# Kernel tuning notes

Hardware: AMD Instinct MI355X
Metric: run time of the kernel (lower is better)

## Reference

```python
import jax, jax.numpy as jnp
import numpy as np

B, F, H, M, T = 4096, 256, 256, 3, 30
IN0 = 2 + F  # GRU layer-0 input: concat(current_pos[2], context[F])


def setup_inputs() -> dict:
    key = jax.random.key(0)
    ks = jax.random.split(key, 15)
    s = 0.05
    rn = lambda k, shp: jax.random.normal(k, shp, jnp.float32) * s
    return dict(
        context=jax.random.normal(ks[0], (B, F), jnp.float32),
        mp_w1=rn(ks[1], (64, F)), mp_b1=rn(ks[2], (64,)),
        mp_w2=rn(ks[3], (M, 64)), mp_b2=rn(ks[4], (M,)),
        w_ih0=rn(ks[5], (M, 3 * H, IN0)), w_hh0=rn(ks[6], (M, 3 * H, H)),
        b_ih0=rn(ks[7], (M, 3 * H)), b_hh0=rn(ks[8], (M, 3 * H)),
        w_ih1=rn(ks[9], (M, 3 * H, H)), w_hh1=rn(ks[10], (M, 3 * H, H)),
        b_ih1=rn(ks[11], (M, 3 * H)), b_hh1=rn(ks[12], (M, 3 * H)),
        out_w=rn(ks[13], (M, 2, H)), out_b=rn(ks[14], (M, 2)),
        num_future_steps=T,
    )


def _gru_cell(x, h, w_ih, w_hh, b_ih, b_hh):
    # PyTorch GRU cell, gate order (r, z, n)
    gx = x @ w_ih.T + b_ih  # (B, 3H)
    gh = h @ w_hh.T + b_hh  # (B, 3H)
    xr, xz, xn = jnp.split(gx, 3, axis=-1)
    hr, hz, hn = jnp.split(gh, 3, axis=-1)
    r = jax.nn.sigmoid(xr + hr)
    z = jax.nn.sigmoid(xz + hz)
    n = jnp.tanh(xn + r * hn)
    return (1.0 - z) * n + z * h


def reference(context, mp_w1, mp_b1, mp_w2, mp_b2,
              w_ih0, w_hh0, b_ih0, b_hh0,
              w_ih1, w_hh1, b_ih1, b_hh1,
              out_w, out_b, num_future_steps):
    mode_logits = jax.nn.relu(context @ mp_w1.T + mp_b1) @ mp_w2.T + mp_b2
    mode_probs = jax.nn.softmax(mode_logits, axis=-1)  # (B, M)

    def decode_mode(wi0, wh0, bi0, bh0, wi1, wh1, bi1, bh1, ow, ob):
        def step(carry, _):
            h0, h1, pos = carry
            x = jnp.concatenate([pos, context], axis=-1)  # (B, 2+F)
            h0n = _gru_cell(x, h0, wi0, wh0, bi0, bh0)
            h1n = _gru_cell(h0n, h1, wi1, wh1, bi1, bh1)
            delta = h1n @ ow.T + ob  # (B, 2)
            return (h0n, h1n, delta), delta

        pos0 = jnp.zeros((context.shape[0], 2), context.dtype)
        # hidden = context.unsqueeze(0).repeat(2,1,1): both layers init to context
        (_, _, _), deltas = jax.lax.scan(step, (context, context, pos0), None,
                                          length=num_future_steps)
        # deltas: (T, B, 2) -> (B, T, 2), cumulative sum over time
        return jnp.cumsum(deltas.transpose(1, 0, 2), axis=1)

    trajs = jax.vmap(decode_mode)(w_ih0, w_hh0, b_ih0, b_hh0,
                                  w_ih1, w_hh1, b_ih1, b_hh1,
                                  out_w, out_b)  # (M, B, T, 2)
    trajectories = trajs.transpose(1, 0, 2, 3)  # (B, M, T, 2)
    return trajectories, mode_probs
```

## Files before the change

kernel.cpp:

```cpp
#include <hip/hip_runtime.h>


typedef __attribute__((ext_vector_type(8))) short bf16x8;
typedef __attribute__((ext_vector_type(4))) float f32x4;

__device__ __forceinline__ short f2bf(float f) {
    unsigned u = __builtin_bit_cast(unsigned, f);
    unsigned r = (u + 0x7fffu + ((u >> 16) & 1u)) >> 16;
    return (short)r;
}
__device__ __forceinline__ float bf2f(short s) {
    unsigned u = ((unsigned)(unsigned short)s) << 16;
    return __builtin_bit_cast(float, u);
}
__device__ __forceinline__ float fast_sigmoid(float x) {
    x = fminf(fmaxf(x, -30.f), 30.f);
    float e = __builtin_amdgcn_exp2f(x * -1.442695041f);
    return __builtin_amdgcn_rcpf(1.f + e);
}
__device__ __forceinline__ float fast_tanh(float x) {
    x = fminf(fmaxf(x, -15.f), 15.f);
    float e = __builtin_amdgcn_exp2f(x * -2.885390082f);
    return (1.f - e) * __builtin_amdgcn_rcpf(1.f + e);
}

__global__ void prep_kernel(const float* __restrict__ w_ih0,
                            const float* __restrict__ w_hh0,
                            const float* __restrict__ w_ih1,
                            const float* __restrict__ w_hh1,
                            short* __restrict__ ws) {
    int bid = blockIdx.x;
    int L = threadIdx.x;
    const float* src;
    int srcRowLen, colBase, m, w, ks, t;
    if (bid < 1152) {
        int idx = bid, mw = idx / 48, blk = idx % 48;
        m = mw / 8; w = mw % 8;
        if (blk < 32) { ks = blk >> 2; t = blk & 3; }
        else { int q = blk - 32; ks = q >> 1; t = 4 + (q & 1); }
        src = w_hh0 + (size_t)m * 768 * 256; srcRowLen = 256; colBase = 0;
    } else if (bid < 3456) {
        int idx = bid - 1152, mw = idx / 96, blk = idx % 96;
        m = mw / 8; w = mw % 8;
        int half;
        if (blk < 64) { half = blk >> 5; ks = (blk >> 2) & 7; t = blk & 3; }
        else { int q = blk - 64; half = q >> 4; ks = (q >> 1) & 7; t = 4 + (q & 1); }
        src = (half ? w_hh1 : w_ih1) + (size_t)m * 768 * 256;
        srcRowLen = 256; colBase = 0;
    } else {
        int idx = bid - 3456, mw = idx / 48, blk = idx % 48;
        m = mw / 8; w = mw % 8; ks = blk / 6; t = blk % 6;
        src = w_ih0 + (size_t)m * 768 * 258; srcRowLen = 258; colBase = 2;
    }
    int row = (t >> 1) * 256 + 32 * w + (t & 1) * 16 + (L & 15);
    int col0 = colBase + ks * 32 + (L >> 4) * 8;
    short* dst = ws + (size_t)bid * 512 + L * 8;
    const float* s = src + (size_t)row * srcRowLen + col0;
#pragma unroll
    for (int j = 0; j < 8; ++j) dst[j] = f2bf(s[j]);
}

__global__ __launch_bounds__(256) void modeprobs_kernel(
    const float* __restrict__ ctx, const float* __restrict__ w1,
    const float* __restrict__ b1, const float* __restrict__ w2,
    const float* __restrict__ b2, float* __restrict__ out,
    long probs_off) {
    __shared__ float w1s[64 * 256];
    int tid = threadIdx.x;
    int j = tid & 63;
    int rsub = tid >> 6;
#pragma unroll
    for (int i = 0; i < 64; ++i) w1s[tid + i * 256] = w1[tid + i * 256];
    float b1v = b1[j];
    float w2v0 = w2[j], w2v1 = w2[64 + j], w2v2 = w2[128 + j];
    float b20 = b2[0], b21 = b2[1], b22 = b2[2];
    __syncthreads();
    for (int c = 0; c < 16; ++c) {
        int brow = blockIdx.x * 64 + c * 4 + rsub;
        const float* crow = ctx + (size_t)brow * 256;
        float accv = b1v;
#pragma unroll 8
        for (int k = 0; k < 256; ++k) {
            int kk = (k + j) & 255;
            accv += w1s[j * 256 + kk] * crow[kk];
        }
        float h = fmaxf(accv, 0.f);
        float l0 = h * w2v0, l1 = h * w2v1, l2 = h * w2v2;
#pragma unroll
        for (int s = 1; s < 64; s <<= 1) {
            l0 += __shfl_xor(l0, s);
            l1 += __shfl_xor(l1, s);
            l2 += __shfl_xor(l2, s);
        }
        if (j == 0) {
            l0 += b20; l1 += b21; l2 += b22;
            float mx = fmaxf(l0, fmaxf(l1, l2));
            float e0 = __builtin_amdgcn_exp2f((l0 - mx) * 1.442695041f);
            float e1 = __builtin_amdgcn_exp2f((l1 - mx) * 1.442695041f);
            float e2 = __builtin_amdgcn_exp2f((l2 - mx) * 1.442695041f);
            float inv = 1.f / (e0 + e1 + e2);
            out[probs_off + (size_t)brow * 3 + 0] = e0 * inv;
            out[probs_off + (size_t)brow * 3 + 1] = e1 * inv;
            out[probs_off + (size_t)brow * 3 + 2] = e2 * inv;
        }
    }
}

__global__ __launch_bounds__(512, 2) void decoder_kernel(
    const float* __restrict__ context,
    const float* __restrict__ w_ih0_f,
    const float* __restrict__ b_ih0, const float* __restrict__ b_hh0,
    const float* __restrict__ b_ih1, const float* __restrict__ b_hh1,
    const float* __restrict__ out_w, const float* __restrict__ out_b,
    const short* __restrict__ ws, float* __restrict__ out,
    const int* __restrict__ pT, int ntiles) {
    __shared__ short ctxS[64 * 264];
    __shared__ short h0a[64 * 264], h0b[64 * 264];
    __shared__ short h1s[64 * 264];
    __shared__ float posD[128];
    __shared__ float owl[512];
    __shared__ float cwp0[768], cwp1[768];
    __shared__ float cbA[512];
    __shared__ float cbXn[256];
    __shared__ float cbh0n[256];
    __shared__ float cb1A[512];
    __shared__ float cb1X[256];
    __shared__ float cb1H[256];

    const int bid = blockIdx.x;
    const int xcd = bid & 7, slot = bid >> 3;
    int mode, xl, nx;
    if (xcd < 3)      { mode = 0; xl = xcd;     nx = 3; }
    else if (xcd < 6) { mode = 1; xl = xcd - 3; nx = 3; }
    else              { mode = 2; xl = xcd - 6; nx = 2; }
    const int g = slot * nx + xl;
    if (g >= ntiles) return;
    const int m = mode;
    const int b0 = g * 64;

    const int T = *pT;
    const int tid = threadIdx.x;
    const int lane = tid & 63, w = tid >> 6;
    const int lr = lane & 15, quad = lane >> 4;

    if (tid < 128) posD[tid] = 0.f;
    owl[tid] = out_w[m * 512 + tid];
    if (tid < 512) {
        cbA[tid] = b_ih0[m * 768 + tid] + b_hh0[m * 768 + tid];
        cb1A[tid] = b_ih1[m * 768 + tid] + b_hh1[m * 768 + tid];
    }
    if (tid < 256) {
        cbXn[tid] = b_ih0[m * 768 + 512 + tid];
        cbh0n[tid] = b_hh0[m * 768 + 512 + tid];
        cb1X[tid] = b_ih1[m * 768 + 512 + tid];
        cb1H[tid] = b_hh1[m * 768 + 512 + tid];
    }
    for (int c = tid; c < 768; c += 512) {
        cwp0[c] = w_ih0_f[((size_t)m * 768 + c) * 258 + 0];
        cwp1[c] = w_ih0_f[((size_t)m * 768 + c) * 258 + 1];
    }
#pragma unroll
    for (int i = 0; i < 32; ++i) {
        int idx = tid + i * 512;
        int r = idx >> 8, k = idx & 255;
        short v = f2bf(context[(size_t)(b0 + r) * 256 + k]);
        ctxS[r * 264 + k] = v;
        h0a[r * 264 + k] = v;
        h1s[r * 264 + k] = v;
    }
    const float ob0v = out_b[m * 2 + 0], ob1v = out_b[m * 2 + 1];

    const short* p0w = ws + ((size_t)(m * 8 + w) * 48) * 512 + lane * 8;
    const short* p1w = ws + (size_t)1152 * 512 + ((size_t)(m * 8 + w) * 96) * 512 + lane * 8;
    const short* pcw = ws + (size_t)3456 * 512 + ((size_t)(m * 8 + w) * 48) * 512 + lane * 8;

    const int cA = 32 * w + lr;
    const int cB = 32 * w + 16 + lr;

    __syncthreads();

    float cum0 = 0.f, cum1 = 0.f;

    for (int st = 0; st < T; ++st) {
        const short* h0c = (st & 1) ? h0b : h0a;
        short* h0n_ = (st & 1) ? h0a : h0b;

        {
            f32x4 arz[4][4], axn[2][4], ahn[2][4];
#pragma unroll
            for (int rt = 0; rt < 4; ++rt)
#pragma unroll
                for (int r = 0; r < 4; ++r) {
                    int row = rt * 16 + quad * 4 + r;
                    float px = posD[row * 2], py = posD[row * 2 + 1];
#pragma unroll
                    for (int t = 0; t < 4; ++t) {
                        int c = (t >> 1) * 256 + ((t & 1) ? cB : cA);
                        arz[t][rt][r] = cbA[c] + px * cwp0[c] + py * cwp1[c];
                    }
#pragma unroll
                    for (int nt = 0; nt < 2; ++nt) {
                        int cn = nt ? cB : cA;
                        axn[nt][rt][r] = cbXn[cn] + px * cwp0[512 + cn] +
                                         py * cwp1[512 + cn];
                        ahn[nt][rt][r] = cbh0n[cn];
                    }
                }
            const short* bpc = pcw;
            const short* bp0rz = p0w;
            const short* bp0n = p0w + 32 * 512;
#pragma unroll 1
            for (int ks = 0; ks < 8; ++ks) {
                bf16x8 ac[4], ah[4];
#pragma unroll
                for (int rt = 0; rt < 4; ++rt) {
                    ac[rt] = *reinterpret_cast<const bf16x8*>(
                        ctxS + (rt * 16 + lr) * 264 + ks * 32 + quad * 8);
                    ah[rt] = *reinterpret_cast<const bf16x8*>(
                        h0c + (rt * 16 + lr) * 264 + ks * 32 + quad * 8);
                }
#pragma unroll
                for (int t = 0; t < 4; ++t) {
                    bf16x8 b = *reinterpret_cast<const bf16x8*>(bpc + t * 512);
#pragma unroll
                    for (int rt = 0; rt < 4; ++rt)
                        arz[t][rt] = __builtin_amdgcn_mfma_f32_16x16x32_bf16(
                            ac[rt], b, arz[t][rt], 0, 0, 0);
                }
#pragma unroll
                for (int nt = 0; nt < 2; ++nt) {
                    bf16x8 b = *reinterpret_cast<const bf16x8*>(bpc + (4 + nt) * 512);
#pragma unroll
                    for (int rt = 0; rt < 4; ++rt)
                        axn[nt][rt] = __builtin_amdgcn_mfma_f32_16x16x32_bf16(
                            ac[rt], b, axn[nt][rt], 0, 0, 0);
                }
#pragma unroll
                for (int t = 0; t < 4; ++t) {
                    bf16x8 b = *reinterpret_cast<const bf16x8*>(bp0rz + t * 512);
#pragma unroll
                    for (int rt = 0; rt < 4; ++rt)
                        arz[t][rt] = __builtin_amdgcn_mfma_f32_16x16x32_bf16(
                            ah[rt], b, arz[t][rt], 0, 0, 0);
                }
#pragma unroll
                for (int nt = 0; nt < 2; ++nt) {
                    bf16x8 b = *reinterpret_cast<const bf16x8*>(bp0n + nt * 512);
#pragma unroll
                    for (int rt = 0; rt < 4; ++rt)
                        ahn[nt][rt] = __builtin_amdgcn_mfma_f32_16x16x32_bf16(
                            ah[rt], b, ahn[nt][rt], 0, 0, 0);
                }
                bpc += 6 * 512;
                bp0rz += 4 * 512;
                bp0n += 2 * 512;
            }
#pragma unroll
            for (int nt = 0; nt < 2; ++nt) {
                int col = nt ? cB : cA;
#pragma unroll
                for (int rt = 0; rt < 4; ++rt)
#pragma unroll
                    for (int r = 0; r < 4; ++r) {
                        int row = rt * 16 + quad * 4 + r;
                        float rr = fast_sigmoid(arz[nt][rt][r]);
                        float zz = fast_sigmoid(arz[2 + nt][rt][r]);
                        float nn =
                            fast_tanh(axn[nt][rt][r] + rr * ahn[nt][rt][r]);
                        float hold = bf2f(h0c[row * 264 + col]);
                        h0n_[row * 264 + col] = f2bf((1.f - zz) * nn + zz * hold);
                    }
            }
        }
        __syncthreads();

        {
            f32x4 arz[4][4], axn[2][4], ahn[2][4];
#pragma unroll
            for (int rt = 0; rt < 4; ++rt)
#pragma unroll
                for (int r = 0; r < 4; ++r) {
#pragma unroll
                    for (int t = 0; t < 4; ++t) {
                        int c = (t >> 1) * 256 + ((t & 1) ? cB : cA);
                        arz[t][rt][r] = cb1A[c];
                    }
#pragma unroll
                    for (int nt = 0; nt < 2; ++nt) {
                        int cn = nt ? cB : cA;
                        axn[nt][rt][r] = cb1X[cn];
                        ahn[nt][rt][r] = cb1H[cn];
                    }
                }
            const short* bq0 = p1w;
            const short* bq1 = p1w + 32 * 512;
            const short* bx = p1w + 64 * 512;
            const short* bh = p1w + 80 * 512;
#pragma unroll 1
            for (int ks = 0; ks < 8; ++ks) {
                bf16x8 a0[4], a1[4];
#pragma unroll
                for (int rt = 0; rt < 4; ++rt) {
                    a0[rt] = *reinterpret_cast<const bf16x8*>(
                        h0n_ + (rt * 16 + lr) * 264 + ks * 32 + quad * 8);
                    a1[rt] = *reinterpret_cast<const bf16x8*>(
                        h1s + (rt * 16 + lr) * 264 + ks * 32 + quad * 8);
                }
#pragma unroll
                for (int t = 0; t < 4; ++t) {
                    bf16x8 b = *reinterpret_cast<const bf16x8*>(bq0 + t * 512);
#pragma unroll
                    for (int rt = 0; rt < 4; ++rt)
                        arz[t][rt] = __builtin_amdgcn_mfma_f32_16x16x32_bf16(
                            a0[rt], b, arz[t][rt], 0, 0, 0);
                }
#pragma unroll
                for (int nt = 0; nt < 2; ++nt) {
                    bf16x8 b = *reinterpret_cast<const bf16x8*>(bx + nt * 512);
#pragma unroll
                    for (int rt = 0; rt < 4; ++rt)
                        axn[nt][rt] = __builtin_amdgcn_mfma_f32_16x16x32_bf16(
                            a0[rt], b, axn[nt][rt], 0, 0, 0);
                }
#pragma unroll
                for (int t = 0; t < 4; ++t) {
                    bf16x8 b = *reinterpret_cast<const bf16x8*>(bq1 + t * 512);
#pragma unroll
                    for (int rt = 0; rt < 4; ++rt)
                        arz[t][rt] = __builtin_amdgcn_mfma_f32_16x16x32_bf16(
                            a1[rt], b, arz[t][rt], 0, 0, 0);
                }
#pragma unroll
                for (int nt = 0; nt < 2; ++nt) {
                    bf16x8 b = *reinterpret_cast<const bf16x8*>(bh + nt * 512);
#pragma unroll
                    for (int rt = 0; rt < 4; ++rt)
                        ahn[nt][rt] = __builtin_amdgcn_mfma_f32_16x16x32_bf16(
                            a1[rt], b, ahn[nt][rt], 0, 0, 0);
                }
                bq0 += 4 * 512;
                bq1 += 4 * 512;
                bx += 2 * 512;
                bh += 2 * 512;
            }
            __syncthreads();
#pragma unroll
            for (int nt = 0; nt < 2; ++nt) {
                int col = nt ? cB : cA;
#pragma unroll
                for (int rt = 0; rt < 4; ++rt)
#pragma unroll
                    for (int r = 0; r < 4; ++r) {
                        int row = rt * 16 + quad * 4 + r;
                        float rr = fast_sigmoid(arz[nt][rt][r]);
                        float zz = fast_sigmoid(arz[2 + nt][rt][r]);
                        float nn =
                            fast_tanh(axn[nt][rt][r] + rr * ahn[nt][rt][r]);
                        float hold = bf2f(h1s[row * 264 + col]);
                        h1s[row * 264 + col] = f2bf((1.f - zz) * nn + zz * hold);
                    }
            }
        }
        __syncthreads();

        {
            int brow = tid >> 3, p = tid & 7;
            float d0 = 0.f, d1 = 0.f;
#pragma unroll
            for (int j = 0; j < 4; ++j) {
                int cb = ((p + brow) & 7) * 8 + j * 64;
                bf16x8 hv8 = *reinterpret_cast<const bf16x8*>(h1s + brow * 264 + cb);
#pragma unroll
                for (int i = 0; i < 8; ++i) {
                    float hv = bf2f(hv8[i]);
                    d0 += hv * owl[cb + i];
                    d1 += hv * owl[256 + cb + i];
                }
            }
            d0 += __shfl_xor(d0, 1); d0 += __shfl_xor(d0, 2); d0 += __shfl_xor(d0, 4);
            d1 += __shfl_xor(d1, 1); d1 += __shfl_xor(d1, 2); d1 += __shfl_xor(d1, 4);
            d0 += ob0v;
            d1 += ob1v;
            if (p == 0) {
                cum0 += d0;
                cum1 += d1;
                size_t o = (((size_t)(b0 + brow) * 3 + m) * (size_t)T + st) * 2;
                out[o] = cum0;
                out[o + 1] = cum1;
                posD[brow * 2] = d0;
                posD[brow * 2 + 1] = d1;
            }
        }
        __syncthreads();
    }
}

extern "C" void kernel_launch(void* const* d_in, const int* in_sizes, int n_in,
                              void* d_out, int out_size, void* d_ws, size_t ws_size,
                              hipStream_t stream) {
    const float* context = (const float*)d_in[0];
    const float* mp_w1 = (const float*)d_in[1];
    const float* mp_b1 = (const float*)d_in[2];
    const float* mp_w2 = (const float*)d_in[3];
    const float* mp_b2 = (const float*)d_in[4];
    const float* w_ih0 = (const float*)d_in[5];
    const float* w_hh0 = (const float*)d_in[6];
    const float* b_ih0 = (const float*)d_in[7];
    const float* b_hh0 = (const float*)d_in[8];
    const float* w_ih1 = (const float*)d_in[9];
    const float* w_hh1 = (const float*)d_in[10];
    const float* b_ih1 = (const float*)d_in[11];
    const float* b_hh1 = (const float*)d_in[12];
    const float* out_w = (const float*)d_in[13];
    const float* out_b = (const float*)d_in[14];
    const int* pT = (const int*)d_in[15];
    float* out = (float*)d_out;
    short* ws = (short*)d_ws;

    const int B = in_sizes[0] / 256;
    const int ntiles = B / 64;
    const long probs_off = (long)out_size - (long)B * 3;

    prep_kernel<<<4608, 64, 0, stream>>>(w_ih0, w_hh0, w_ih1, w_hh1, ws);
    modeprobs_kernel<<<B / 64, 256, 0, stream>>>(context, mp_w1, mp_b1, mp_w2,
                                                 mp_b2, out, probs_off);
    const int nslots = (ntiles + 1) / 2;
    decoder_kernel<<<8 * nslots, 512, 0, stream>>>(
        context, w_ih0, b_ih0, b_hh0, b_ih1, b_hh1, out_w, out_b, ws, out, pT,
        ntiles);
}
```

Baseline: 976.4 us.

## Split GRU gate GEMMs into r/z and n passes with double-buffered weight loads

Each GRU layer's fused K-loop, which kept r/z and n accumulators live together, is split into two passes. The r/z pass applies sigmoid right away and keeps the results as floats, then the n pass runs with only its own accumulators. Each pass double-buffers the global weight fragments so the next K-slice's B operands load while the current MFMAs run. This is meant to lower accumulator register pressure and hide global load latency, at the cost of reading the A operands from LDS twice per step and holding extra rv/zv registers.

```diff
diff --git a/kernel.cpp b/kernel.cpp
--- a/kernel.cpp
+++ b/kernel.cpp
@@ -106,6 +106,71 @@
     }
 }
 
+__device__ __forceinline__ void load_rz(bf16x8 (&bu)[8], const short* pX,
+                                        const short* pY, int offX, int offY) {
+#pragma unroll
+    for (int t = 0; t < 4; ++t) {
+        bu[t] = *reinterpret_cast<const bf16x8*>(pX + offX + t * 512);
+        bu[4 + t] = *reinterpret_cast<const bf16x8*>(pY + offY + t * 512);
+    }
+}
+__device__ __forceinline__ void mfma_rz(f32x4 (&acc)[4][4], const bf16x8 (&bu)[8],
+                                        const short* aP, const short* bP,
+                                        int kk, int lr, int quad) {
+    bf16x8 a0[4], a1[4];
+#pragma unroll
+    for (int rt = 0; rt < 4; ++rt) {
+        a0[rt] = *reinterpret_cast<const bf16x8*>(
+            aP + (rt * 16 + lr) * 264 + kk * 32 + quad * 8);
+        a1[rt] = *reinterpret_cast<const bf16x8*>(
+            bP + (rt * 16 + lr) * 264 + kk * 32 + quad * 8);
+    }
+#pragma unroll
+    for (int t = 0; t < 4; ++t)
+#pragma unroll
+        for (int rt = 0; rt < 4; ++rt)
+            acc[t][rt] = __builtin_amdgcn_mfma_f32_16x16x32_bf16(
+                a0[rt], bu[t], acc[t][rt], 0, 0, 0);
+#pragma unroll
+    for (int t = 0; t < 4; ++t)
+#pragma unroll
+        for (int rt = 0; rt < 4; ++rt)
+            acc[t][rt] = __builtin_amdgcn_mfma_f32_16x16x32_bf16(
+                a1[rt], bu[4 + t], acc[t][rt], 0, 0, 0);
+}
+__device__ __forceinline__ void load_n(bf16x8 (&bu)[4], const short* pX,
+                                       const short* pY, int offX, int offY) {
+#pragma unroll
+    for (int t = 0; t < 2; ++t) {
+        bu[t] = *reinterpret_cast<const bf16x8*>(pX + offX + t * 512);
+        bu[2 + t] = *reinterpret_cast<const bf16x8*>(pY + offY + t * 512);
+    }
+}
+__device__ __forceinline__ void mfma_n(f32x4 (&ax)[2][4], f32x4 (&ah)[2][4],
+                                       const bf16x8 (&bu)[4], const short* aP,
+                                       const short* bP, int kk, int lr, int quad) {
+    bf16x8 a0[4], a1[4];
+#pragma unroll
+    for (int rt = 0; rt < 4; ++rt) {
+        a0[rt] = *reinterpret_cast<const bf16x8*>(
+            aP + (rt * 16 + lr) * 264 + kk * 32 + quad * 8);
+        a1[rt] = *reinterpret_cast<const bf16x8*>(
+            bP + (rt * 16 + lr) * 264 + kk * 32 + quad * 8);
+    }
+#pragma unroll
+    for (int nt = 0; nt < 2; ++nt)
+#pragma unroll
+        for (int rt = 0; rt < 4; ++rt)
+            ax[nt][rt] = __builtin_amdgcn_mfma_f32_16x16x32_bf16(
+                a0[rt], bu[nt], ax[nt][rt], 0, 0, 0);
+#pragma unroll
+    for (int nt = 0; nt < 2; ++nt)
+#pragma unroll
+        for (int rt = 0; rt < 4; ++rt)
+            ah[nt][rt] = __builtin_amdgcn_mfma_f32_16x16x32_bf16(
+                a1[rt], bu[2 + nt], ah[nt][rt], 0, 0, 0);
+}
+
 __global__ __launch_bounds__(512, 2) void decoder_kernel(
     const float* __restrict__ context,
     const float* __restrict__ w_ih0_f,
@@ -155,9 +220,9 @@
         cb1X[tid] = b_ih1[m * 768 + 512 + tid];
         cb1H[tid] = b_hh1[m * 768 + 512 + tid];
     }
-    for (int c = tid; c < 768; c += 512) {
-        cwp0[c] = w_ih0_f[((size_t)m * 768 + c) * 258 + 0];
-        cwp1[c] = w_ih0_f[((size_t)m * 768 + c) * 258 + 1];
+    for (int cc = tid; cc < 768; cc += 512) {
+        cwp0[cc] = w_ih0_f[((size_t)m * 768 + cc) * 258 + 0];
+        cwp1[cc] = w_ih0_f[((size_t)m * 768 + cc) * 258 + 1];
     }
 #pragma unroll
     for (int i = 0; i < 32; ++i) {
@@ -173,6 +238,10 @@
     const short* p0w = ws + ((size_t)(m * 8 + w) * 48) * 512 + lane * 8;
     const short* p1w = ws + (size_t)1152 * 512 + ((size_t)(m * 8 + w) * 96) * 512 + lane * 8;
     const short* pcw = ws + (size_t)3456 * 512 + ((size_t)(m * 8 + w) * 48) * 512 + lane * 8;
+    const short* p0n = p0w + 32 * 512;
+    const short* p1x = p1w + 64 * 512;
+    const short* p1h = p1w + 80 * 512;
+    const short* p1q = p1w + 32 * 512;
 
     const int cA = 32 * w + lr;
     const int cB = 32 * w + 16 + lr;
@@ -185,8 +254,9 @@
         const short* h0c = (st & 1) ? h0b : h0a;
         short* h0n_ = (st & 1) ? h0a : h0b;
 
+        float rv[2][4][4], zv[2][4][4];
         {
-            f32x4 arz[4][4], axn[2][4], ahn[2][4];
+            f32x4 arz[4][4];
 #pragma unroll
             for (int rt = 0; rt < 4; ++rt)
 #pragma unroll
@@ -198,6 +268,38 @@
                         int c = (t >> 1) * 256 + ((t & 1) ? cB : cA);
                         arz[t][rt][r] = cbA[c] + px * cwp0[c] + py * cwp1[c];
                     }
+                }
+            {
+                bf16x8 bu0[8], bu1[8];
+                load_rz(bu0, pcw, p0w, 0, 0);
+#pragma unroll 1
+                for (int ks2 = 0; ks2 < 4; ++ks2) {
+                    int k0 = 2 * ks2, k1 = k0 + 1, k2 = k0 + 2;
+                    load_rz(bu1, pcw, p0w, k1 * 6 * 512, k1 * 4 * 512);
+                    mfma_rz(arz, bu0, ctxS, h0c, k0, lr, quad);
+                    if (ks2 < 3)
+                        load_rz(bu0, pcw, p0w, k2 * 6 * 512, k2 * 4 * 512);
+                    mfma_rz(arz, bu1, ctxS, h0c, k1, lr, quad);
+                }
+            }
+#pragma unroll
+            for (int nt = 0; nt < 2; ++nt)
+#pragma unroll
+                for (int rt = 0; rt < 4; ++rt)
+#pragma unroll
+                    for (int r = 0; r < 4; ++r) {
+                        rv[nt][rt][r] = fast_sigmoid(arz[nt][rt][r]);
+                        zv[nt][rt][r] = fast_sigmoid(arz[2 + nt][rt][r]);
+                    }
+        }
+        {
+            f32x4 axn[2][4], ahn[2][4];
+#pragma unroll
+            for (int rt = 0; rt < 4; ++rt)
+#pragma unroll
+                for (int r = 0; r < 4; ++r) {
+                    int row = rt * 16 + quad * 4 + r;
+                    float px = posD[row * 2], py = posD[row * 2 + 1];
 #pragma unroll
                     for (int nt = 0; nt < 2; ++nt) {
                         int cn = nt ? cB : cA;
@@ -206,54 +308,18 @@
                         ahn[nt][rt][r] = cbh0n[cn];
                     }
                 }
-            const short* bpc = pcw;
-            const short* bp0rz = p0w;
-            const short* bp0n = p0w + 32 * 512;
+            {
+                bf16x8 bu0[4], bu1[4];
+                load_n(bu0, pcw, p0n, 4 * 512, 0);
 #pragma unroll 1
-            for (int ks = 0; ks < 8; ++ks) {
-                bf16x8 ac[4], ah[4];
-#pragma unroll
-                for (int rt = 0; rt < 4; ++rt) {
-                    ac[rt] = *reinterpret_cast<const bf16x8*>(
-                        ctxS + (rt * 16 + lr) * 264 + ks * 32 + quad * 8);
-                    ah[rt] = *reinterpret_cast<const bf16x8*>(
-                        h0c + (rt * 16 + lr) * 264 + ks * 32 + quad * 8);
-                }
-#pragma unroll
-                for (int t = 0; t < 4; ++t) {
-                    bf16x8 b = *reinterpret_cast<const bf16x8*>(bpc + t * 512);
-#pragma unroll
-                    for (int rt = 0; rt < 4; ++rt)
-                        arz[t][rt] = __builtin_amdgcn_mfma_f32_16x16x32_bf16(
-                            ac[rt], b, arz[t][rt], 0, 0, 0);
-                }
-#pragma unroll
-                for (int nt = 0; nt < 2; ++nt) {
-                    bf16x8 b = *reinterpret_cast<const bf16x8*>(bpc + (4 + nt) * 512);
-#pragma unroll
-                    for (int rt = 0; rt < 4; ++rt)
-                        axn[nt][rt] = __builtin_amdgcn_mfma_f32_16x16x32_bf16(
-                            ac[rt], b, axn[nt][rt], 0, 0, 0);
-                }
-#pragma unroll
-                for (int t = 0; t < 4; ++t) {
-                    bf16x8 b = *reinterpret_cast<const bf16x8*>(bp0rz + t * 512);
-#pragma unroll
-                    for (int rt = 0; rt < 4; ++rt)
-                        arz[t][rt] = __builtin_amdgcn_mfma_f32_16x16x32_bf16(
-                            ah[rt], b, arz[t][rt], 0, 0, 0);
-                }
-#pragma unroll
-                for (int nt = 0; nt < 2; ++nt) {
-                    bf16x8 b = *reinterpret_cast<const bf16x8*>(bp0n + nt * 512);
-#pragma unroll
-                    for (int rt = 0; rt < 4; ++rt)
-                        ahn[nt][rt] = __builtin_amdgcn_mfma_f32_16x16x32_bf16(
-                            ah[rt], b, ahn[nt][rt], 0, 0, 0);
-                }
-                bpc += 6 * 512;
-                bp0rz += 4 * 512;
-                bp0n += 2 * 512;
+                for (int ks2 = 0; ks2 < 4; ++ks2) {
+                    int k0 = 2 * ks2, k1 = k0 + 1, k2 = k0 + 2;
+                    load_n(bu1, pcw, p0n, (k1 * 6 + 4) * 512, k1 * 2 * 512);
+                    mfma_n(axn, ahn, bu0, ctxS, h0c, k0, lr, quad);
+                    if (ks2 < 3)
+                        load_n(bu0, pcw, p0n, (k2 * 6 + 4) * 512, k2 * 2 * 512);
+                    mfma_n(axn, ahn, bu1, ctxS, h0c, k1, lr, quad);
+                }
             }
 #pragma unroll
             for (int nt = 0; nt < 2; ++nt) {
@@ -263,85 +329,75 @@
 #pragma unroll
                     for (int r = 0; r < 4; ++r) {
                         int row = rt * 16 + quad * 4 + r;
-                        float rr = fast_sigmoid(arz[nt][rt][r]);
-                        float zz = fast_sigmoid(arz[2 + nt][rt][r]);
-                        float nn =
-                            fast_tanh(axn[nt][rt][r] + rr * ahn[nt][rt][r]);
+                        float nn = fast_tanh(axn[nt][rt][r] +
+                                             rv[nt][rt][r] * ahn[nt][rt][r]);
                         float hold = bf2f(h0c[row * 264 + col]);
-                        h0n_[row * 264 + col] = f2bf((1.f - zz) * nn + zz * hold);
+                        h0n_[row * 264 + col] =
+                            f2bf((1.f - zv[nt][rt][r]) * nn +
+                                 zv[nt][rt][r] * hold);
                     }
             }
         }
         __syncthreads();
 
         {
-            f32x4 arz[4][4], axn[2][4], ahn[2][4];
+            f32x4 arz[4][4];
 #pragma unroll
             for (int rt = 0; rt < 4; ++rt)
 #pragma unroll
-                for (int r = 0; r < 4; ++r) {
+                for (int r = 0; r < 4; ++r)
 #pragma unroll
                     for (int t = 0; t < 4; ++t) {
                         int c = (t >> 1) * 256 + ((t & 1) ? cB : cA);
                         arz[t][rt][r] = cb1A[c];
                     }
+            {
+                bf16x8 bu0[8], bu1[8];
+                load_rz(bu0, p1w, p1q, 0, 0);
+#pragma unroll 1
+                for (int ks2 = 0; ks2 < 4; ++ks2) {
+                    int k0 = 2 * ks2, k1 = k0 + 1, k2 = k0 + 2;
+                    load_rz(bu1, p1w, p1q, k1 * 4 * 512, k1 * 4 * 512);
+                    mfma_rz(arz, bu0, h0n_, h1s, k0, lr, quad);
+                    if (ks2 < 3)
+                        load_rz(bu0, p1w, p1q, k2 * 4 * 512, k2 * 4 * 512);
+                    mfma_rz(arz, bu1, h0n_, h1s, k1, lr, quad);
+                }
+            }
+#pragma unroll
+            for (int nt = 0; nt < 2; ++nt)
+#pragma unroll
+                for (int rt = 0; rt < 4; ++rt)
+#pragma unroll
+                    for (int r = 0; r < 4; ++r) {
+                        rv[nt][rt][r] = fast_sigmoid(arz[nt][rt][r]);
+                        zv[nt][rt][r] = fast_sigmoid(arz[2 + nt][rt][r]);
+                    }
+        }
+        {
+            f32x4 axn[2][4], ahn[2][4];
+#pragma unroll
+            for (int rt = 0; rt < 4; ++rt)
+#pragma unroll
+                for (int r = 0; r < 4; ++r)
 #pragma unroll
                     for (int nt = 0; nt < 2; ++nt) {
                         int cn = nt ? cB : cA;
                         axn[nt][rt][r] = cb1X[cn];
                         ahn[nt][rt][r] = cb1H[cn];
                     }
-                }
-            const short* bq0 = p1w;
-            const short* bq1 = p1w + 32 * 512;
-            const short* bx = p1w + 64 * 512;
-            const short* bh = p1w + 80 * 512;
+            {
+                bf16x8 bu0[4], bu1[4];
+                load_n(bu0, p1x, p1h, 0, 0);
 #pragma unroll 1
-            for (int ks = 0; ks < 8; ++ks) {
-                bf16x8 a0[4], a1[4];
-#pragma unroll
-                for (int rt = 0; rt < 4; ++rt) {
-                    a0[rt] = *reinterpret_cast<const bf16x8*>(
-                        h0n_ + (rt * 16 + lr) * 264 + ks * 32 + quad * 8);
-                    a1[rt] = *reinterpret_cast<const bf16x8*>(
-                        h1s + (rt * 16 + lr) * 264 + ks * 32 + quad * 8);
-                }
-#pragma unroll
-                for (int t = 0; t < 4; ++t) {
-                    bf16x8 b = *reinterpret_cast<const bf16x8*>(bq0 + t * 512);
-#pragma unroll
-                    for (int rt = 0; rt < 4; ++rt)
-                        arz[t][rt] = __builtin_amdgcn_mfma_f32_16x16x32_bf16(
-                            a0[rt], b, arz[t][rt], 0, 0, 0);
-                }
-#pragma unroll
-                for (int nt = 0; nt < 2; ++nt) {
-                    bf16x8 b = *reinterpret_cast<const bf16x8*>(bx + nt * 512);
-#pragma unroll
-                    for (int rt = 0; rt < 4; ++rt)
-                        axn[nt][rt] = __builtin_amdgcn_mfma_f32_16x16x32_bf16(
-                            a0[rt], b, axn[nt][rt], 0, 0, 0);
-                }
-#pragma unroll
-                for (int t = 0; t < 4; ++t) {
-                    bf16x8 b = *reinterpret_cast<const bf16x8*>(bq1 + t * 512);
-#pragma unroll
-                    for (int rt = 0; rt < 4; ++rt)
-                        arz[t][rt] = __builtin_amdgcn_mfma_f32_16x16x32_bf16(
-                            a1[rt], b, arz[t][rt], 0, 0, 0);
-                }
-#pragma unroll
-                for (int nt = 0; nt < 2; ++nt) {
-                    bf16x8 b = *reinterpret_cast<const bf16x8*>(bh + nt * 512);
-#pragma unroll
-                    for (int rt = 0; rt < 4; ++rt)
-                        ahn[nt][rt] = __builtin_amdgcn_mfma_f32_16x16x32_bf16(
-                            a1[rt], b, ahn[nt][rt], 0, 0, 0);
-                }
-                bq0 += 4 * 512;
-                bq1 += 4 * 512;
-                bx += 2 * 512;
-                bh += 2 * 512;
+                for (int ks2 = 0; ks2 < 4; ++ks2) {
+                    int k0 = 2 * ks2, k1 = k0 + 1, k2 = k0 + 2;
+                    load_n(bu1, p1x, p1h, k1 * 2 * 512, k1 * 2 * 512);
+                    mfma_n(axn, ahn, bu0, h0n_, h1s, k0, lr, quad);
+                    if (ks2 < 3)
+                        load_n(bu0, p1x, p1h, k2 * 2 * 512, k2 * 2 * 512);
+                    mfma_n(axn, ahn, bu1, h0n_, h1s, k1, lr, quad);
+                }
             }
             __syncthreads();
 #pragma unroll
@@ -352,12 +408,12 @@
 #pragma unroll
                     for (int r = 0; r < 4; ++r) {
                         int row = rt * 16 + quad * 4 + r;
-                        float rr = fast_sigmoid(arz[nt][rt][r]);
-                        float zz = fast_sigmoid(arz[2 + nt][rt][r]);
-                        float nn =
-                            fast_tanh(axn[nt][rt][r] + rr * ahn[nt][rt][r]);
+                        float nn = fast_tanh(axn[nt][rt][r] +
+                                             rv[nt][rt][r] * ahn[nt][rt][r]);
                         float hold = bf2f(h1s[row * 264 + col]);
-                        h1s[row * 264 + col] = f2bf((1.f - zz) * nn + zz * hold);
+                        h1s[row * 264 + col] =
+                            f2bf((1.f - zv[nt][rt][r]) * nn +
+                                 zv[nt][rt][r] * hold);
                     }
             }
         }
```

After: 1.142 ms. 16.9% more time.

## Stream GRU weights through per-wave LDS staging with async global_load_lds prefetch

Applied to the files above, without the earlier changes.

Weight B-fragments are no longer loaded straight from global memory into registers. Each wave now prefetches the next group of three fragments into its own LDS staging buffer with global_load_lds, and uses vmcnt waits to overlap those loads with the current group's MFMAs, carrying the prefetch chain across the layer-0 and layer-1 phases and across timesteps. The h0 double buffer is folded into a single buffer, and several bias and position-weight tables are stored as bf16 so the larger staging area still fits in LDS. This adds fragile manual waitcnt and barrier handling, and the bf16 biases introduce extra rounding.

```diff
diff --git a/kernel.cpp b/kernel.cpp
--- a/kernel.cpp
+++ b/kernel.cpp
@@ -106,6 +106,41 @@
     }
 }
 
+__device__ __forceinline__ void gl16(const short* g, short* l) {
+    __builtin_amdgcn_global_load_lds(
+        (const __attribute__((address_space(1))) unsigned int*)g,
+        (__attribute__((address_space(3))) unsigned int*)l, 16, 0, 0);
+}
+__device__ __forceinline__ void barrier_lgkm() {
+    asm volatile("s_waitcnt lgkmcnt(0)" ::: "memory");
+    __builtin_amdgcn_s_barrier();
+}
+__device__ __forceinline__ void phase3(const short* rbuf,
+                                       const short* i0, const short* i1,
+                                       const short* i2,
+                                       short* wbuf,
+                                       const bf16x8 (&a)[4], f32x4 (&A0)[4],
+                                       f32x4 (&A1)[4], f32x4 (&A2)[4]) {
+    asm volatile("s_waitcnt vmcnt(3)" ::: "memory");
+    bf16x8 b0 = *reinterpret_cast<const bf16x8*>(rbuf);
+    bf16x8 b1 = *reinterpret_cast<const bf16x8*>(rbuf + 512);
+    bf16x8 b2 = *reinterpret_cast<const bf16x8*>(rbuf + 1024);
+    asm volatile("s_waitcnt lgkmcnt(0)" ::: "memory");
+    __builtin_amdgcn_sched_barrier(0);
+    gl16(i0, wbuf);
+    gl16(i1, wbuf + 512);
+    gl16(i2, wbuf + 1024);
+#pragma unroll
+    for (int rt = 0; rt < 4; ++rt)
+        A0[rt] = __builtin_amdgcn_mfma_f32_16x16x32_bf16(a[rt], b0, A0[rt], 0, 0, 0);
+#pragma unroll
+    for (int rt = 0; rt < 4; ++rt)
+        A1[rt] = __builtin_amdgcn_mfma_f32_16x16x32_bf16(a[rt], b1, A1[rt], 0, 0, 0);
+#pragma unroll
+    for (int rt = 0; rt < 4; ++rt)
+        A2[rt] = __builtin_amdgcn_mfma_f32_16x16x32_bf16(a[rt], b2, A2[rt], 0, 0, 0);
+}
+
 __global__ __launch_bounds__(512, 2) void decoder_kernel(
     const float* __restrict__ context,
     const float* __restrict__ w_ih0_f,
@@ -115,17 +150,16 @@
     const short* __restrict__ ws, float* __restrict__ out,
     const int* __restrict__ pT, int ntiles) {
     __shared__ short ctxS[64 * 264];
-    __shared__ short h0a[64 * 264], h0b[64 * 264];
+    __shared__ short h0s[64 * 264];
     __shared__ short h1s[64 * 264];
+    __shared__ short stg[8 * 3072];
     __shared__ float posD[128];
     __shared__ float owl[512];
-    __shared__ float cwp0[768], cwp1[768];
+    __shared__ short cwp0h[768], cwp1h[768];
     __shared__ float cbA[512];
-    __shared__ float cbXn[256];
-    __shared__ float cbh0n[256];
     __shared__ float cb1A[512];
-    __shared__ float cb1X[256];
-    __shared__ float cb1H[256];
+    __shared__ short cbXn[256], cbh0n[256];
+    __shared__ short cb1X[256], cb1H[256];
 
     const int bid = blockIdx.x;
     const int xcd = bid & 7, slot = bid >> 3;
@@ -145,19 +179,17 @@
 
     if (tid < 128) posD[tid] = 0.f;
     owl[tid] = out_w[m * 512 + tid];
-    if (tid < 512) {
-        cbA[tid] = b_ih0[m * 768 + tid] + b_hh0[m * 768 + tid];
-        cb1A[tid] = b_ih1[m * 768 + tid] + b_hh1[m * 768 + tid];
-    }
+    cbA[tid] = b_ih0[m * 768 + tid] + b_hh0[m * 768 + tid];
+    cb1A[tid] = b_ih1[m * 768 + tid] + b_hh1[m * 768 + tid];
     if (tid < 256) {
-        cbXn[tid] = b_ih0[m * 768 + 512 + tid];
-        cbh0n[tid] = b_hh0[m * 768 + 512 + tid];
-        cb1X[tid] = b_ih1[m * 768 + 512 + tid];
-        cb1H[tid] = b_hh1[m * 768 + 512 + tid];
-    }
-    for (int c = tid; c < 768; c += 512) {
-        cwp0[c] = w_ih0_f[((size_t)m * 768 + c) * 258 + 0];
-        cwp1[c] = w_ih0_f[((size_t)m * 768 + c) * 258 + 1];
+        cbXn[tid] = f2bf(b_ih0[m * 768 + 512 + tid]);
+        cbh0n[tid] = f2bf(b_hh0[m * 768 + 512 + tid]);
+        cb1X[tid] = f2bf(b_ih1[m * 768 + 512 + tid]);
+        cb1H[tid] = f2bf(b_hh1[m * 768 + 512 + tid]);
+    }
+    for (int cc = tid; cc < 768; cc += 512) {
+        cwp0h[cc] = f2bf(w_ih0_f[((size_t)m * 768 + cc) * 258 + 0]);
+        cwp1h[cc] = f2bf(w_ih0_f[((size_t)m * 768 + cc) * 258 + 1]);
     }
 #pragma unroll
     for (int i = 0; i < 32; ++i) {
@@ -165,7 +197,7 @@
         int r = idx >> 8, k = idx & 255;
         short v = f2bf(context[(size_t)(b0 + r) * 256 + k]);
         ctxS[r * 264 + k] = v;
-        h0a[r * 264 + k] = v;
+        h0s[r * 264 + k] = v;
         h1s[r * 264 + k] = v;
     }
     const float ob0v = out_b[m * 2 + 0], ob1v = out_b[m * 2 + 1];
@@ -173,18 +205,29 @@
     const short* p0w = ws + ((size_t)(m * 8 + w) * 48) * 512 + lane * 8;
     const short* p1w = ws + (size_t)1152 * 512 + ((size_t)(m * 8 + w) * 96) * 512 + lane * 8;
     const short* pcw = ws + (size_t)3456 * 512 + ((size_t)(m * 8 + w) * 48) * 512 + lane * 8;
+    const short* p0n = p0w + 32 * 512;
+    const short* p1q = p1w + 32 * 512;
+    const short* p1x = p1w + 64 * 512;
+    const short* p1h = p1w + 80 * 512;
+
+    short* stgW = stg + w * 3072;
+    const short* stgR = stgW + lane * 8;
 
     const int cA = 32 * w + lr;
     const int cB = 32 * w + 16 + lr;
 
     __syncthreads();
 
+    gl16(pcw, stgW);
+    gl16(pcw + 512, stgW + 512);
+    gl16(pcw + 2 * 512, stgW + 2 * 512);
+    gl16(pcw + 3 * 512, stgW + 1536);
+    gl16(pcw + 4 * 512, stgW + 1536 + 512);
+    gl16(pcw + 5 * 512, stgW + 1536 + 1024);
+
     float cum0 = 0.f, cum1 = 0.f;
 
     for (int st = 0; st < T; ++st) {
-        const short* h0c = (st & 1) ? h0b : h0a;
-        short* h0n_ = (st & 1) ? h0a : h0b;
-
         {
             f32x4 arz[4][4], axn[2][4], ahn[2][4];
 #pragma unroll
@@ -196,65 +239,48 @@
 #pragma unroll
                     for (int t = 0; t < 4; ++t) {
                         int c = (t >> 1) * 256 + ((t & 1) ? cB : cA);
-                        arz[t][rt][r] = cbA[c] + px * cwp0[c] + py * cwp1[c];
+                        arz[t][rt][r] = cbA[c] + px * bf2f(cwp0h[c]) +
+                                        py * bf2f(cwp1h[c]);
                     }
 #pragma unroll
                     for (int nt = 0; nt < 2; ++nt) {
                         int cn = nt ? cB : cA;
-                        axn[nt][rt][r] = cbXn[cn] + px * cwp0[512 + cn] +
-                                         py * cwp1[512 + cn];
-                        ahn[nt][rt][r] = cbh0n[cn];
+                        axn[nt][rt][r] = bf2f(cbXn[cn]) +
+                                         px * bf2f(cwp0h[512 + cn]) +
+                                         py * bf2f(cwp1h[512 + cn]);
+                        ahn[nt][rt][r] = bf2f(cbh0n[cn]);
                     }
                 }
-            const short* bpc = pcw;
-            const short* bp0rz = p0w;
-            const short* bp0n = p0w + 32 * 512;
+            const short* ih = p0w;
+            const short* in_ = p0n;
+            const short* ic = pcw + 6 * 512;
 #pragma unroll 1
             for (int ks = 0; ks < 8; ++ks) {
                 bf16x8 ac[4], ah[4];
 #pragma unroll
-                for (int rt = 0; rt < 4; ++rt) {
+                for (int rt = 0; rt < 4; ++rt)
                     ac[rt] = *reinterpret_cast<const bf16x8*>(
                         ctxS + (rt * 16 + lr) * 264 + ks * 32 + quad * 8);
+                phase3(stgR, ih, ih + 512, ih + 2 * 512, stgW, ac,
+                       arz[0], arz[1], arz[2]);
+                phase3(stgR + 1536, ih + 3 * 512, in_, in_ + 512, stgW + 1536,
+                       ac, arz[3], axn[0], axn[1]);
+#pragma unroll
+                for (int rt = 0; rt < 4; ++rt)
                     ah[rt] = *reinterpret_cast<const bf16x8*>(
-                        h0c + (rt * 16 + lr) * 264 + ks * 32 + quad * 8);
-                }
-#pragma unroll
-                for (int t = 0; t < 4; ++t) {
-                    bf16x8 b = *reinterpret_cast<const bf16x8*>(bpc + t * 512);
-#pragma unroll
-                    for (int rt = 0; rt < 4; ++rt)
-                        arz[t][rt] = __builtin_amdgcn_mfma_f32_16x16x32_bf16(
-                            ac[rt], b, arz[t][rt], 0, 0, 0);
-                }
-#pragma unroll
-                for (int nt = 0; nt < 2; ++nt) {
-                    bf16x8 b = *reinterpret_cast<const bf16x8*>(bpc + (4 + nt) * 512);
-#pragma unroll
-                    for (int rt = 0; rt < 4; ++rt)
-                        axn[nt][rt] = __builtin_amdgcn_mfma_f32_16x16x32_bf16(
-                            ac[rt], b, axn[nt][rt], 0, 0, 0);
-                }
-#pragma unroll
-                for (int t = 0; t < 4; ++t) {
-                    bf16x8 b = *reinterpret_cast<const bf16x8*>(bp0rz + t * 512);
-#pragma unroll
-                    for (int rt = 0; rt < 4; ++rt)
-                        arz[t][rt] = __builtin_amdgcn_mfma_f32_16x16x32_bf16(
-                            ah[rt], b, arz[t][rt], 0, 0, 0);
-                }
-#pragma unroll
-                for (int nt = 0; nt < 2; ++nt) {
-                    bf16x8 b = *reinterpret_cast<const bf16x8*>(bp0n + nt * 512);
-#pragma unroll
-                    for (int rt = 0; rt < 4; ++rt)
-                        ahn[nt][rt] = __builtin_amdgcn_mfma_f32_16x16x32_bf16(
-                            ah[rt], b, ahn[nt][rt], 0, 0, 0);
-                }
-                bpc += 6 * 512;
-                bp0rz += 4 * 512;
-                bp0n += 2 * 512;
-            }
+                        h0s + (rt * 16 + lr) * 264 + ks * 32 + quad * 8);
+                const short* nA = (ks < 7) ? ic : p1w;
+                const short* nB0 = (ks < 7) ? ic + 4 * 512 : p1x;
+                const short* nB1 = (ks < 7) ? ic + 5 * 512 : p1x + 512;
+                phase3(stgR, nA, nA + 512, nA + 2 * 512, stgW, ah,
+                       arz[0], arz[1], arz[2]);
+                phase3(stgR + 1536, nA + 3 * 512, nB0, nB1, stgW + 1536, ah,
+                       arz[3], ahn[0], ahn[1]);
+                ih += 4 * 512;
+                in_ += 2 * 512;
+                ic += 6 * 512;
+            }
+            barrier_lgkm();
 #pragma unroll
             for (int nt = 0; nt < 2; ++nt) {
                 int col = nt ? cB : cA;
@@ -267,12 +293,12 @@
                         float zz = fast_sigmoid(arz[2 + nt][rt][r]);
                         float nn =
                             fast_tanh(axn[nt][rt][r] + rr * ahn[nt][rt][r]);
-                        float hold = bf2f(h0c[row * 264 + col]);
-                        h0n_[row * 264 + col] = f2bf((1.f - zz) * nn + zz * hold);
-                    }
-            }
-        }
-        __syncthreads();
+                        float hold = bf2f(h0s[row * 264 + col]);
+                        h0s[row * 264 + col] = f2bf((1.f - zz) * nn + zz * hold);
+                    }
+            }
+        }
+        barrier_lgkm();
 
         {
             f32x4 arz[4][4], axn[2][4], ahn[2][4];
@@ -288,62 +314,42 @@
 #pragma unroll
                     for (int nt = 0; nt < 2; ++nt) {
                         int cn = nt ? cB : cA;
-                        axn[nt][rt][r] = cb1X[cn];
-                        ahn[nt][rt][r] = cb1H[cn];
+                        axn[nt][rt][r] = bf2f(cb1X[cn]);
+                        ahn[nt][rt][r] = bf2f(cb1H[cn]);
                     }
                 }
-            const short* bq0 = p1w;
-            const short* bq1 = p1w + 32 * 512;
-            const short* bx = p1w + 64 * 512;
-            const short* bh = p1w + 80 * 512;
+            const short* iq1 = p1q;
+            const short* iy = p1h;
+            const short* iq0 = p1w + 4 * 512;
+            const short* ix = p1x + 2 * 512;
 #pragma unroll 1
             for (int ks = 0; ks < 8; ++ks) {
                 bf16x8 a0[4], a1[4];
 #pragma unroll
-                for (int rt = 0; rt < 4; ++rt) {
+                for (int rt = 0; rt < 4; ++rt)
                     a0[rt] = *reinterpret_cast<const bf16x8*>(
-                        h0n_ + (rt * 16 + lr) * 264 + ks * 32 + quad * 8);
+                        h0s + (rt * 16 + lr) * 264 + ks * 32 + quad * 8);
+                phase3(stgR, iq1, iq1 + 512, iq1 + 2 * 512, stgW, a0,
+                       arz[0], arz[1], arz[2]);
+                phase3(stgR + 1536, iq1 + 3 * 512, iy, iy + 512, stgW + 1536,
+                       a0, arz[3], axn[0], axn[1]);
+#pragma unroll
+                for (int rt = 0; rt < 4; ++rt)
                     a1[rt] = *reinterpret_cast<const bf16x8*>(
                         h1s + (rt * 16 + lr) * 264 + ks * 32 + quad * 8);
-                }
-#pragma unroll
-                for (int t = 0; t < 4; ++t) {
-                    bf16x8 b = *reinterpret_cast<const bf16x8*>(bq0 + t * 512);
-#pragma unroll
-                    for (int rt = 0; rt < 4; ++rt)
-                        arz[t][rt] = __builtin_amdgcn_mfma_f32_16x16x32_bf16(
-                            a0[rt], b, arz[t][rt], 0, 0, 0);
-                }
-#pragma unroll
-                for (int nt = 0; nt < 2; ++nt) {
-                    bf16x8 b = *reinterpret_cast<const bf16x8*>(bx + nt * 512);
-#pragma unroll
-                    for (int rt = 0; rt < 4; ++rt)
-                        axn[nt][rt] = __builtin_amdgcn_mfma_f32_16x16x32_bf16(
-                            a0[rt], b, axn[nt][rt], 0, 0, 0);
-                }
-#pragma unroll
-                for (int t = 0; t < 4; ++t) {
-                    bf16x8 b = *reinterpret_cast<const bf16x8*>(bq1 + t * 512);
-#pragma unroll
-                    for (int rt = 0; rt < 4; ++rt)
-                        arz[t][rt] = __builtin_amdgcn_mfma_f32_16x16x32_bf16(
-                            a1[rt], b, arz[t][rt], 0, 0, 0);
-                }
-#pragma unroll
-                for (int nt = 0; nt < 2; ++nt) {
-                    bf16x8 b = *reinterpret_cast<const bf16x8*>(bh + nt * 512);
-#pragma unroll
-                    for (int rt = 0; rt < 4; ++rt)
-                        ahn[nt][rt] = __builtin_amdgcn_mfma_f32_16x16x32_bf16(
-                            a1[rt], b, ahn[nt][rt], 0, 0, 0);
-                }
-                bq0 += 4 * 512;
-                bq1 += 4 * 512;
-                bx += 2 * 512;
-                bh += 2 * 512;
-            }
-            __syncthreads();
+                const short* mA = (ks < 7) ? iq0 : pcw;
+                const short* mB0 = (ks < 7) ? ix : pcw + 4 * 512;
+                const short* mB1 = (ks < 7) ? ix + 512 : pcw + 5 * 512;
+                phase3(stgR, mA, mA + 512, mA + 2 * 512, stgW, a1,
+                       arz[0], arz[1], arz[2]);
+                phase3(stgR + 1536, mA + 3 * 512, mB0, mB1, stgW + 1536, a1,
+                       arz[3], ahn[0], ahn[1]);
+                iq1 += 4 * 512;
+                iy += 2 * 512;
+                iq0 += 4 * 512;
+                ix += 2 * 512;
+            }
+            barrier_lgkm();
 #pragma unroll
             for (int nt = 0; nt < 2; ++nt) {
                 int col = nt ? cB : cA;
@@ -361,7 +367,7 @@
                     }
             }
         }
-        __syncthreads();
+        barrier_lgkm();
 
         {
             int brow = tid >> 3, p = tid & 7;
@@ -391,8 +397,9 @@
                 posD[brow * 2 + 1] = d1;
             }
         }
-        __syncthreads();
-    }
+        barrier_lgkm();
+    }
+    asm volatile("s_waitcnt vmcnt(0)" ::: "memory");
 }
 
 extern "C" void kernel_launch(void* const* d_in, const int* in_sizes, int n_in,
```

Result: no change. 988.1 us (+1.2%).
